# Performance work log

Hardware: AMD Instinct MI355X
Metric: run time of the kernel (lower is better)

## Reference

```python
import jax, jax.numpy as jnp
import numpy as np

N = 100000   # total nodes across the batch
D = 3        # ambient dimension of the point cloud
T = 64       # num_thetas (directions)
R = 64       # resolution of the ECT discretization
B = 128      # number of point clouds in the batch
RADIUS = 1.1
SCALE = 8.0


def setup_inputs() -> dict:
    key = jax.random.key(0)
    kx, kv, kb = jax.random.split(key, 3)
    x = jax.random.normal(kx, (N, D), dtype=jnp.float32)
    # directions; the layer stores v movedim'd and moves it back, so math uses [D, T]
    v = jax.random.normal(kv, (D, T), dtype=jnp.float32)
    v = v / jnp.linalg.norm(v, axis=0, keepdims=True)  # unit directions, typical usage
    batch = jnp.sort(jax.random.randint(kb, (N,), 0, B, dtype=jnp.int64))
    return {"x": x, "v": v, "batch": batch}


def reference(x, v, batch):
    # compute_ect_points:
    # nh[n,t] = <x_n, v_t>
    nh = x @ v  # [N, T]
    lin = jnp.linspace(-RADIUS, RADIUS, R, dtype=x.dtype)  # [R]
    # ecc[n,t,r] = sigmoid(scale * (lin[r] - nh[n,t]))  -- large [N,T,R] intermediate
    ecc = jax.nn.sigmoid(SCALE * (lin[None, None, :] - nh[:, :, None]))
    # scatter-sum over the batch index (index_add): -> [B, T, R]
    ect = jax.ops.segment_sum(ecc, batch, num_segments=B)
    # normalized=False -> return ect.squeeze(); no singleton dims here
    return ect
```

## Files before the change

kernel.cpp:

```cpp
#include <hip/hip_runtime.h>
#include <math.h>


#define THREADS 256
#define TPB 4
#define TQ  16
#define J0  64
#define STEPS 144
#define ROWW 128
#define HO_BASE (TPB * ROWW)
#define HF_BASE (2 * TPB * ROWW)
#define ROW32 256
#define BSEG 128

#if __has_builtin(__builtin_amdgcn_fmed3f)
#define CLAMP(v, lo, hi) __builtin_amdgcn_fmed3f((v), (lo), (hi))
#else
#define CLAMP(v, lo, hi) fminf(fmaxf((v), (lo)), (hi))
#endif

constexpr double cexp_taylor(double r) {
    double s = 1.0, term = 1.0;
    for (int i = 1; i < 18; ++i) { term *= r / (double)i; s += term; }
    return s;
}
constexpr double cexp(double x) {
    const double LN2 = 0.69314718055994530942;
    const int n = (int)(x / LN2 + (x >= 0.0 ? 0.5 : -0.5));
    const double r = x - (double)n * LN2;
    double e = cexp_taylor(r);
    if (n >= 0) { for (int i = 0; i < n;  ++i) e *= 2.0; }
    else        { for (int i = 0; i < -n; ++i) e *= 0.5; }
    return e;
}
struct WTab {
    float w[STEPS];
    constexpr WTab() : w() {
        const double d = 2.2 / 63.0;
        for (int j = 0; j < STEPS; ++j) {
            const double z = 8.0 * d * (double)(111 - j);
            w[j] = (float)(1.0 / ((1.0 + cexp(-z)) * 256.0));
        }
    }
};
constexpr WTab WT;

__device__ __forceinline__ float wave_suffix(float x, int lane) {
#pragma unroll
    for (int d = 1; d < 64; d <<= 1) {
        const float y = __shfl_down(x, d, 64);
        x += (lane + d < 64) ? y : 0.0f;
    }
    return x;
}

__device__ __forceinline__ int lower_scalar(const int* __restrict__ A, int n,
                                            int val) {
    const long long g = ((long long)val * (long long)n) >> 7;
    int lo = (int)(g - 1024 > 0 ? g - 1024 : 0);
    int hi = (int)(g + 1024 < n ? g + 1024 : n);
    const bool okl = (lo == 0) || (A[__builtin_amdgcn_readfirstlane(lo - 1)] < val);
    const bool okh = (hi == n) || (A[__builtin_amdgcn_readfirstlane(hi)] >= val);
    if (!(okl && okh)) { lo = 0; hi = n; }
    while (hi > lo) {
        const int mid = (lo + hi) >> 1;
        const int key = A[__builtin_amdgcn_readfirstlane(mid)];
        if (key < val) lo = mid + 1; else hi = mid;
    }
    return lo;
}

__global__ __launch_bounds__(THREADS, 8) void ect_fused11_kernel(
    const float* __restrict__ x,
    const float* __restrict__ v,
    const int*   __restrict__ batch,
    float* __restrict__ out,
    int n, float inv_d256, float bias256)
{
    __shared__ unsigned Ls[2 * TPB * ROWW + TPB * ROW32];

    const int tid  = threadIdx.x;
    const int wv   = tid >> 6;
    const int lane = tid & 63;
    const int b    = blockIdx.x >> 4;
    const int tq   = blockIdx.x & (TQ - 1);

    {
        unsigned long long* z = (unsigned long long*)Ls;
        for (int i = tid; i < TPB * ROWW; i += THREADS) z[i] = 0ull;
    }

    const int s0 = lower_scalar(batch, n, b);
    const int s1 = lower_scalar(batch, n, b + 1);

    const int t_l  = lane >> 4;
    const int slot = (lane & 15) + (wv << 4);
    const int tbase = tq * TPB;
    const int t    = tbase + t_l;
    const float va = v[t], vb = v[64 + t], vc = v[128 + t];
    const int rowbyte = (t_l * ROWW) << 2;

    __syncthreads();

#define DEPOSIT(x0, x1, x2)                                                   \
    {                                                                         \
        const float nh = fmaf((x0), va, fmaf((x1), vb, (x2) * vc));           \
        float bf = fmaf(nh, inv_d256, bias256);                               \
        bf = CLAMP(bf, 16128.0f, 56831.0f);               \
        const unsigned ufix = (unsigned)bf;      \
        const unsigned q1   = ufix & 255u;                                    \
        const unsigned val  = (q1 << 16) + (256u - q1);                       \
        const unsigned wbyte = ((ufix >> 7) & ~3u)             \
                             + ((ufix >> 6) & 4u ? (HO_BASE << 2) : 0u)       \
                             + rowbyte;                                       \
        atomicAdd((unsigned*)((char*)Ls + wbyte), val);                       \
    }

    {
        const int len = s1 - s0;
        const int nfull = len >> 8;
        int base = s0;
        for (int c = 0; c < nfull; ++c, base += 256) {
            float xs[4][3];
#pragma unroll
            for (int k = 0; k < 4; ++k) {
                const float3 xx = *(const float3*)(x + 3 * (size_t)(base + (k << 6) + slot));
                xs[k][0] = xx.x; xs[k][1] = xx.y; xs[k][2] = xx.z;
            }
#pragma unroll
            for (int k = 0; k < 4; ++k) DEPOSIT(xs[k][0], xs[k][1], xs[k][2]);
        }
        for (; base < s1; base += 64) {
            const int idx = base + slot;
            if (idx < s1) {
                const float3 xx = *(const float3*)(x + 3 * (size_t)idx);
                DEPOSIT(xx.x, xx.y, xx.z);
            }
        }
    }

    __syncthreads();

    float c[4];
    {
        const unsigned* He = Ls + wv * ROWW;
        const unsigned* Ho = Ls + HO_BASE + wv * ROWW;
        float* Hf = (float*)(Ls + HF_BASE) + wv * ROW32;
        const int par = lane & 1;
#pragma unroll
        for (int q = 0; q < 4; ++q) {
            const int a = lane + 64 * q;
            const unsigned heW = He[a >> 1];
            const unsigned he  = par ? (heW >> 16) : (heW & 0xFFFFu);
            unsigned ho = 0u;
            if (a > 0) {
                const unsigned hoW = Ho[(a - 1) >> 1];
                ho = par ? (hoW & 0xFFFFu) : (hoW >> 16);
            }
            c[q] = (float)(he + ho);
            if (q > 0) Hf[a] = c[q];
        }
    }

    float tot23 = c[2] + c[3];
#pragma unroll
    for (int d = 1; d < 64; d <<= 1) tot23 += __shfl_xor(tot23, d, 64);
    const float s1v   = wave_suffix(c[1], lane) + tot23;
    const float carry = __shfl(s1v, 0, 64);
    const float s0v   = wave_suffix(c[0], lane) + carry;
    const float window = (s0v - s1v) * (1.0f / 256.0f);

    __syncthreads();

    const float* H = (const float*)(Ls + HF_BASE) + wv * ROW32 + lane;
    float a0 = window, a1 = 0.f;
#pragma unroll
    for (int j = J0; j < STEPS; j += 2) {
        a0 = fmaf(WT.w[j],     H[j],     a0);
        a1 = fmaf(WT.w[j + 1], H[j + 1], a1);
    }
    out[((size_t)b * 64 + tbase + wv) * 64 + lane] = a0 + a1;
#undef DEPOSIT
}

extern "C" void kernel_launch(void* const* d_in, const int* in_sizes, int n_in,
                              void* d_out, int out_size, void* d_ws, size_t ws_size,
                              hipStream_t stream) {
    const float* x     = (const float*)d_in[0];
    const float* v     = (const float*)d_in[1];
    const int*   batch = (const int*)d_in[2];
    float*       out   = (float*)d_out;

    const int n = in_sizes[0] / 3;

    const double d = 2.2 / 63.0;
    const float inv_d256 = (float)(256.0 / d);
    const float bias256  = (79.5f + 63.0f) * 256.0f;

    hipLaunchKernelGGL(ect_fused11_kernel, dim3(BSEG * TQ), dim3(THREADS), 0,
                       stream, x, v, batch, out, n, inv_d256, bias256);
}
```

Before: 16.15 us.

## Process eight directions per block and halve grid size

Each block now handles 8 directions instead of 4, so each node's coordinates are loaded once for twice as many directions and the batch binary search runs over half as many blocks. Each wave finalizes two histogram rows in the scan and the weighted-sum phases. The deposit address now uses a bitwise OR encoding, matched to the doubled shared-memory histogram layout. The trade-off is more atomic contention per row, since 8 lanes share a row instead of 16, fewer blocks for the scheduler to spread, and longer per-wave epilogue work.

```diff
diff --git a/kernel.cpp b/kernel.cpp
--- a/kernel.cpp
+++ b/kernel.cpp
@@ -3,8 +3,8 @@
 
 
 #define THREADS 256
-#define TPB 4
-#define TQ  16
+#define TPB 8
+#define TQ  8
 #define J0  64
 #define STEPS 144
 #define ROWW 128
@@ -70,7 +70,7 @@
     return lo;
 }
 
-__global__ __launch_bounds__(THREADS, 8) void ect_fused11_kernel(
+__global__ __launch_bounds__(THREADS, 8) void ect_fused12_kernel(
     const float* __restrict__ x,
     const float* __restrict__ v,
     const int*   __restrict__ batch,
@@ -82,7 +82,7 @@
     const int tid  = threadIdx.x;
     const int wv   = tid >> 6;
     const int lane = tid & 63;
-    const int b    = blockIdx.x >> 4;
+    const int b    = blockIdx.x >> 3;
     const int tq   = blockIdx.x & (TQ - 1);
 
     {
@@ -93,12 +93,12 @@
     const int s0 = lower_scalar(batch, n, b);
     const int s1 = lower_scalar(batch, n, b + 1);
 
-    const int t_l  = lane >> 4;
-    const int slot = (lane & 15) + (wv << 4);
+    const int t_l  = lane >> 3;
+    const int slot = (lane & 7) + (wv << 3);
     const int tbase = tq * TPB;
     const int t    = tbase + t_l;
     const float va = v[t], vb = v[64 + t], vc = v[128 + t];
-    const int rowbyte = (t_l * ROWW) << 2;
+    const int rowbyte = t_l << 9;
 
     __syncthreads();
 
@@ -107,30 +107,30 @@
         const float nh = fmaf((x0), va, fmaf((x1), vb, (x2) * vc));           \
         float bf = fmaf(nh, inv_d256, bias256);                               \
         bf = CLAMP(bf, 16128.0f, 56831.0f);               \
-        const unsigned ufix = (unsigned)bf;      \
+        const unsigned ufix = (unsigned)bf;                                   \
         const unsigned q1   = ufix & 255u;                                    \
         const unsigned val  = (q1 << 16) + (256u - q1);                       \
-        const unsigned wbyte = ((ufix >> 7) & ~3u)             \
-                             + ((ufix >> 6) & 4u ? (HO_BASE << 2) : 0u)       \
-                             + rowbyte;                                       \
+        const unsigned wbyte = ((ufix >> 7) & ~3u)                            \
+                             | ((ufix & 256u) << 4)                           \
+                             | (unsigned)rowbyte;                             \
         atomicAdd((unsigned*)((char*)Ls + wbyte), val);                       \
     }
 
     {
         const int len = s1 - s0;
-        const int nfull = len >> 8;
+        const int nfull = len >> 7;
         int base = s0;
-        for (int c = 0; c < nfull; ++c, base += 256) {
+        for (int c = 0; c < nfull; ++c, base += 128) {
             float xs[4][3];
 #pragma unroll
             for (int k = 0; k < 4; ++k) {
-                const float3 xx = *(const float3*)(x + 3 * (size_t)(base + (k << 6) + slot));
+                const float3 xx = *(const float3*)(x + 3 * (size_t)(base + (k << 5) + slot));
                 xs[k][0] = xx.x; xs[k][1] = xx.y; xs[k][2] = xx.z;
             }
 #pragma unroll
             for (int k = 0; k < 4; ++k) DEPOSIT(xs[k][0], xs[k][1], xs[k][2]);
         }
-        for (; base < s1; base += 64) {
+        for (; base < s1; base += 32) {
             const int idx = base + slot;
             if (idx < s1) {
                 const float3 xx = *(const float3*)(x + 3 * (size_t)idx);
@@ -141,45 +141,64 @@
 
     __syncthreads();
 
-    float c[4];
+    float win[2];
     {
-        const unsigned* He = Ls + wv * ROWW;
-        const unsigned* Ho = Ls + HO_BASE + wv * ROWW;
-        float* Hf = (float*)(Ls + HF_BASE) + wv * ROW32;
         const int par = lane & 1;
 #pragma unroll
-        for (int q = 0; q < 4; ++q) {
-            const int a = lane + 64 * q;
-            const unsigned heW = He[a >> 1];
-            const unsigned he  = par ? (heW >> 16) : (heW & 0xFFFFu);
-            unsigned ho = 0u;
-            if (a > 0) {
-                const unsigned hoW = Ho[(a - 1) >> 1];
-                ho = par ? (hoW & 0xFFFFu) : (hoW >> 16);
+        for (int rr = 0; rr < 2; ++rr) {
+            const int row = 2 * wv + rr;
+            const unsigned* He = Ls + row * ROWW;
+            const unsigned* Ho = Ls + HO_BASE + row * ROWW;
+            float* Hf = (float*)(Ls + HF_BASE) + row * ROW32;
+            float c0, c1, c2, c3;
+            {
+                unsigned heW, he, ho;
+                heW = He[lane >> 1];
+                he  = par ? (heW >> 16) : (heW & 0xFFFFu);
+                ho  = 0u;
+                if (lane > 0) {
+                    const unsigned hoW = Ho[(lane - 1) >> 1];
+                    ho = par ? (hoW & 0xFFFFu) : (hoW >> 16);
+                }
+                c0 = (float)(he + ho);
+                const int a1 = lane + 64, a2 = lane + 128, a3 = lane + 192;
+                heW = He[a1 >> 1]; he = par ? (heW >> 16) : (heW & 0xFFFFu);
+                { const unsigned hoW = Ho[(a1 - 1) >> 1];
+                  ho = par ? (hoW & 0xFFFFu) : (hoW >> 16); }
+                c1 = (float)(he + ho); Hf[a1] = c1;
+                heW = He[a2 >> 1]; he = par ? (heW >> 16) : (heW & 0xFFFFu);
+                { const unsigned hoW = Ho[(a2 - 1) >> 1];
+                  ho = par ? (hoW & 0xFFFFu) : (hoW >> 16); }
+                c2 = (float)(he + ho); Hf[a2] = c2;
+                heW = He[a3 >> 1]; he = par ? (heW >> 16) : (heW & 0xFFFFu);
+                { const unsigned hoW = Ho[(a3 - 1) >> 1];
+                  ho = par ? (hoW & 0xFFFFu) : (hoW >> 16); }
+                c3 = (float)(he + ho); Hf[a3] = c3;
             }
-            c[q] = (float)(he + ho);
-            if (q > 0) Hf[a] = c[q];
-        }
-    }
-
-    float tot23 = c[2] + c[3];
-#pragma unroll
-    for (int d = 1; d < 64; d <<= 1) tot23 += __shfl_xor(tot23, d, 64);
-    const float s1v   = wave_suffix(c[1], lane) + tot23;
-    const float carry = __shfl(s1v, 0, 64);
-    const float s0v   = wave_suffix(c[0], lane) + carry;
-    const float window = (s0v - s1v) * (1.0f / 256.0f);
+            float tot23 = c2 + c3;
+#pragma unroll
+            for (int d = 1; d < 64; d <<= 1) tot23 += __shfl_xor(tot23, d, 64);
+            const float s1v   = wave_suffix(c1, lane) + tot23;
+            const float carry = __shfl(s1v, 0, 64);
+            const float s0v   = wave_suffix(c0, lane) + carry;
+            win[rr] = (s0v - s1v) * (1.0f / 256.0f);
+        }
+    }
 
     __syncthreads();
 
-    const float* H = (const float*)(Ls + HF_BASE) + wv * ROW32 + lane;
-    float a0 = window, a1 = 0.f;
-#pragma unroll
-    for (int j = J0; j < STEPS; j += 2) {
-        a0 = fmaf(WT.w[j],     H[j],     a0);
-        a1 = fmaf(WT.w[j + 1], H[j + 1], a1);
-    }
-    out[((size_t)b * 64 + tbase + wv) * 64 + lane] = a0 + a1;
+#pragma unroll
+    for (int rr = 0; rr < 2; ++rr) {
+        const int row = 2 * wv + rr;
+        const float* H = (const float*)(Ls + HF_BASE) + row * ROW32 + lane;
+        float a0 = win[rr], a1 = 0.f;
+#pragma unroll
+        for (int j = J0; j < STEPS; j += 2) {
+            a0 = fmaf(WT.w[j],     H[j],     a0);
+            a1 = fmaf(WT.w[j + 1], H[j + 1], a1);
+        }
+        out[((size_t)b * 64 + tbase + row) * 64 + lane] = a0 + a1;
+    }
 #undef DEPOSIT
 }
 
@@ -197,6 +216,6 @@
     const float inv_d256 = (float)(256.0 / d);
     const float bias256  = (79.5f + 63.0f) * 256.0f;
 
-    hipLaunchKernelGGL(ect_fused11_kernel, dim3(BSEG * TQ), dim3(THREADS), 0,
+    hipLaunchKernelGGL(ect_fused12_kernel, dim3(BSEG * TQ), dim3(THREADS), 0,
                        stream, x, v, batch, out, n, inv_d256, bias256);
 }
```

Measured after the change: 16.61 us. 2.8% more time.

## Use wave-parallel ballot search for segment bounds and vectorized LDS reads

Applied to the files above, without the earlier changes.

Swaps the serial per-wave binary search for segment boundaries for a two-level ballot search. All 64 lanes probe the guessed window in parallel, first at stride 32 and then at stride 1, with a full binary search kept as a fallback when the guess window is wrong. It also stores a second copy of the histogram shifted by one element, so each lane can read aligned float2 pairs in the final weighted sum, and uses four accumulators. This cuts the chain of dependent global loads at kernel start and halves the LDS read instructions, at the cost of extra LDS space and stores.

```diff
diff --git a/kernel.cpp b/kernel.cpp
--- a/kernel.cpp
+++ b/kernel.cpp
@@ -10,6 +10,7 @@
 #define ROWW 128
 #define HO_BASE (TPB * ROWW)
 #define HF_BASE (2 * TPB * ROWW)
+#define HFS_BASE (HF_BASE + TPB * 256)
 #define ROW32 256
 #define BSEG 128
 
@@ -18,6 +19,8 @@
 #else
 #define CLAMP(v, lo, hi) fminf(fmaxf((v), (lo)), (hi))
 #endif
+
+typedef float f2 __attribute__((ext_vector_type(2)));
 
 constexpr double cexp_taylor(double r) {
     double s = 1.0, term = 1.0;
@@ -54,14 +57,9 @@
     return x;
 }
 
-__device__ __forceinline__ int lower_scalar(const int* __restrict__ A, int n,
-                                            int val) {
-    const long long g = ((long long)val * (long long)n) >> 7;
-    int lo = (int)(g - 1024 > 0 ? g - 1024 : 0);
-    int hi = (int)(g + 1024 < n ? g + 1024 : n);
-    const bool okl = (lo == 0) || (A[__builtin_amdgcn_readfirstlane(lo - 1)] < val);
-    const bool okh = (hi == n) || (A[__builtin_amdgcn_readfirstlane(hi)] >= val);
-    if (!(okl && okh)) { lo = 0; hi = n; }
+__device__ __forceinline__ int lower_fallback(const int* __restrict__ A,
+                                              int n, int val) {
+    int lo = 0, hi = n;
     while (hi > lo) {
         const int mid = (lo + hi) >> 1;
         const int key = A[__builtin_amdgcn_readfirstlane(mid)];
@@ -70,14 +68,36 @@
     return lo;
 }
 
-__global__ __launch_bounds__(THREADS, 8) void ect_fused11_kernel(
+__device__ __forceinline__ int lower_vec(const int* __restrict__ A, int n,
+                                         int val, int lane, bool* bad) {
+    const long long g = ((long long)val * (long long)n) >> 7;
+    int wlo = (int)g - 1024; if (wlo < 0) wlo = 0;
+    int whi = (int)g + 1024; if (whi > n) whi = n;
+    const bool okl = (wlo == 0) || (A[wlo - 1] < val);
+    const bool okh = (whi == n) || (A[whi] >= val);
+    const int p  = wlo + (lane << 5);
+    const int pc = (p < whi) ? p : (whi - 1);
+    const unsigned long long m1 = __ballot((p < whi) && (A[pc] < val));
+    if (!(okl && okh)) { *bad = true; return 0; }
+    const int c1 = __popcll(m1);
+    if (c1 == 0) return wlo;
+    const int lo2 = wlo + ((c1 - 1) << 5) + 1;
+    int hi2 = wlo + (c1 << 5); if (hi2 > whi) hi2 = whi;
+    const int w  = hi2 - lo2;
+    const int q  = lo2 + lane;
+    const int qc = (q < n) ? q : (n - 1);
+    const unsigned long long m2 = __ballot((lane < w) && (A[qc] < val));
+    return lo2 + __popcll(m2);
+}
+
+__global__ __launch_bounds__(THREADS, 8) void ect_fused14_kernel(
     const float* __restrict__ x,
     const float* __restrict__ v,
     const int*   __restrict__ batch,
     float* __restrict__ out,
     int n, float inv_d256, float bias256)
 {
-    __shared__ unsigned Ls[2 * TPB * ROWW + TPB * ROW32];
+    __shared__ unsigned Ls[HFS_BASE + TPB * ROW32];
 
     const int tid  = threadIdx.x;
     const int wv   = tid >> 6;
@@ -90,15 +110,20 @@
         for (int i = tid; i < TPB * ROWW; i += THREADS) z[i] = 0ull;
     }
 
-    const int s0 = lower_scalar(batch, n, b);
-    const int s1 = lower_scalar(batch, n, b + 1);
+    bool bad = false;
+    int s0 = lower_vec(batch, n, b,     lane, &bad);
+    int s1 = lower_vec(batch, n, b + 1, lane, &bad);
+    if (bad) {
+        s0 = lower_fallback(batch, n, b);
+        s1 = lower_fallback(batch, n, b + 1);
+    }
 
     const int t_l  = lane >> 4;
     const int slot = (lane & 15) + (wv << 4);
     const int tbase = tq * TPB;
     const int t    = tbase + t_l;
     const float va = v[t], vb = v[64 + t], vc = v[128 + t];
-    const int rowbyte = (t_l * ROWW) << 2;
+    const int rowbyte = t_l << 9;
 
     __syncthreads();
 
@@ -107,12 +132,12 @@
         const float nh = fmaf((x0), va, fmaf((x1), vb, (x2) * vc));           \
         float bf = fmaf(nh, inv_d256, bias256);                               \
         bf = CLAMP(bf, 16128.0f, 56831.0f);               \
-        const unsigned ufix = (unsigned)bf;      \
+        const unsigned ufix = (unsigned)bf;                                   \
         const unsigned q1   = ufix & 255u;                                    \
         const unsigned val  = (q1 << 16) + (256u - q1);                       \
-        const unsigned wbyte = ((ufix >> 7) & ~3u)             \
-                             + ((ufix >> 6) & 4u ? (HO_BASE << 2) : 0u)       \
-                             + rowbyte;                                       \
+        const unsigned wbyte = ((ufix >> 7) & ~3u)                            \
+                             + ((ufix & 256u) ? (HO_BASE << 2) : 0u)          \
+                             + (unsigned)rowbyte;                             \
         atomicAdd((unsigned*)((char*)Ls + wbyte), val);                       \
     }
 
@@ -145,7 +170,8 @@
     {
         const unsigned* He = Ls + wv * ROWW;
         const unsigned* Ho = Ls + HO_BASE + wv * ROWW;
-        float* Hf = (float*)(Ls + HF_BASE) + wv * ROW32;
+        float* Hf  = (float*)(Ls + HF_BASE)  + wv * ROW32;
+        float* Hfs = (float*)(Ls + HFS_BASE) + wv * ROW32;
         const int par = lane & 1;
 #pragma unroll
         for (int q = 0; q < 4; ++q) {
@@ -158,7 +184,7 @@
                 ho = par ? (hoW & 0xFFFFu) : (hoW >> 16);
             }
             c[q] = (float)(he + ho);
-            if (q > 0) Hf[a] = c[q];
+            if (q > 0) { Hf[a] = c[q]; Hfs[a - 1] = c[q]; }
         }
     }
 
@@ -172,14 +198,21 @@
 
     __syncthreads();
 
-    const float* H = (const float*)(Ls + HF_BASE) + wv * ROW32 + lane;
-    float a0 = window, a1 = 0.f;
-#pragma unroll
-    for (int j = J0; j < STEPS; j += 2) {
-        a0 = fmaf(WT.w[j],     H[j],     a0);
-        a1 = fmaf(WT.w[j + 1], H[j + 1], a1);
-    }
-    out[((size_t)b * 64 + tbase + wv) * 64 + lane] = a0 + a1;
+    const int odd = lane & 1;
+    const float* Hb = (const float*)(Ls + (odd ? HFS_BASE : HF_BASE))
+                      + wv * ROW32 + lane + 64 - odd;
+    const f2* H2 = (const f2*)Hb;
+    float a0 = window, a1 = 0.f, a2 = 0.f, a3 = 0.f;
+#pragma unroll
+    for (int k = 0; k < (STEPS - J0) / 4; ++k) {
+        const f2 u = H2[2 * k];
+        const f2 w2 = H2[2 * k + 1];
+        a0 = fmaf(WT.w[J0 + 4 * k],     u.x,  a0);
+        a1 = fmaf(WT.w[J0 + 4 * k + 1], u.y,  a1);
+        a2 = fmaf(WT.w[J0 + 4 * k + 2], w2.x, a2);
+        a3 = fmaf(WT.w[J0 + 4 * k + 3], w2.y, a3);
+    }
+    out[((size_t)b * 64 + tbase + wv) * 64 + lane] = (a0 + a1) + (a2 + a3);
 #undef DEPOSIT
 }
 
@@ -197,6 +230,6 @@
     const float inv_d256 = (float)(256.0 / d);
     const float bias256  = (79.5f + 63.0f) * 256.0f;
 
-    hipLaunchKernelGGL(ect_fused11_kernel, dim3(BSEG * TQ), dim3(THREADS), 0,
+    hipLaunchKernelGGL(ect_fused14_kernel, dim3(BSEG * TQ), dim3(THREADS), 0,
                        stream, x, v, batch, out, n, inv_d256, bias256);
 }
```

New measurement: 18.20 us. 12.7% more time.
